# Performance work log

Hardware: AMD Instinct MI355X
Metric: run time of the kernel (lower is better)

## Reference

```python
import jax, jax.numpy as jnp
import numpy as np

CONTEXT = 3  # matches init_kwargs

def _shift_fwd(x, d):
    # out[:, d:, :] = x[:, :-d, :] ; zeros in front
    N = x.shape[1]
    return jnp.pad(x, ((0, 0), (d, 0), (0, 0)))[:, :N, :]

def _shift_bwd(x, d):
    # out[:, :-d, :] = x[:, d:, :] ; zeros at end
    return jnp.pad(x, ((0, 0), (0, d), (0, 0)))[:, d:, :]

def _pairing(x_l, x_r, context):
    if context <= 1:
        return x_l, x_r
    # NB: torch source initializes both lists with x_l (faithful reproduction)
    z_l, z_r = [x_l], [x_l]
    for d in range(1, context // 2 + 1):
        z_l.append(_shift_fwd(x_l, d))   # z_lu
        z_r.append(_shift_bwd(x_r, d))   # z_ru
        z_l.append(_shift_bwd(x_l, d))   # z_ld
        z_r.append(_shift_fwd(x_r, d))   # z_rd
    return jnp.concatenate(z_l, axis=2), jnp.concatenate(z_r, axis=2)

def setup_inputs() -> dict:
    key = jax.random.key(0)
    ks = jax.random.split(key, 8)
    B, N, n_in = 2, 512, 64
    n = n_in * CONTEXT  # 192
    H = 128
    n_out = 8
    s = 0.05
    return {
        "x_l": jax.random.normal(ks[0], (B, N, n_in), jnp.float32),
        "x_r": jax.random.normal(ks[1], (B, N, n_in), jnp.float32),
        "fc_l_W": jax.random.normal(ks[2], (H, n), jnp.float32) * s,
        "fc_l_b": jax.random.normal(ks[3], (H,), jnp.float32) * s,
        "fc_r_W": jax.random.normal(ks[4], (H, n), jnp.float32) * s,
        "fc_r_b": jax.random.normal(ks[5], (H,), jnp.float32) * s,
        "bilinear_W": jax.random.normal(ks[6], (n_out, H, H), jnp.float32) * s,
        "bilinear_b": jax.random.normal(ks[7], (n_out,), jnp.float32) * s,
    }

def reference(x_l, x_r, fc_l_W, fc_l_b, fc_r_W, fc_r_b, bilinear_W, bilinear_b):
    # context-shift pairing: [B,N,n_in] -> [B,N,n_in*context]
    zl, zr = _pairing(x_l, x_r, CONTEXT)
    # per-position MLP with CELU (dropout_rate=0 -> identity)
    hl = jax.nn.celu(jnp.einsum('bnf,hf->bnh', zl, fc_l_W) + fc_l_b)
    hr = jax.nn.celu(jnp.einsum('bnf,hf->bnh', zr, fc_r_W) + fc_r_b)
    # bilinear over the NxN pair grid without materializing [B,N,N,H]:
    # out[b,i,j,o] = hl[b,i] @ W[o] @ hr[b,j] + b[o]
    t = jnp.einsum('bih,ohg->biog', hl, bilinear_W)   # [B,N,n_out,H]
    out = jnp.einsum('biog,bjg->bijo', t, hr) + bilinear_b
    return out  # [B,N,N,n_out]
```

## Files before the change

kernel.cpp:

```cpp
#include <hip/hip_runtime.h>
#include <math.h>

#define BB 2
#define NN 512
#define NIN 64
#define NF 192
#define HH 128
#define NOUT 8

typedef short short8 __attribute__((ext_vector_type(8)));
typedef float f32x4 __attribute__((ext_vector_type(4)));

__device__ __forceinline__ float celu1(float x) {
    return x > 0.0f ? x : expm1f(x);
}

__device__ __forceinline__ ushort f2b(float f) {
    union { float f; uint u; } v; v.f = f;
    uint r = v.u + 0x7fffu + ((v.u >> 16) & 1u);
    return (ushort)(r >> 16);
}
__device__ __forceinline__ uint pack2(float a, float b) {
    return (uint)f2b(a) | ((uint)f2b(b) << 16);
}
__device__ __forceinline__ short8 cvt8(const float* __restrict__ p) {
    float4 a = *(const float4*)p;
    float4 b = *(const float4*)(p + 4);
    union { uint4 u; short8 s; } c;
    c.u.x = pack2(a.x, a.y); c.u.y = pack2(a.z, a.w);
    c.u.z = pack2(b.x, b.y); c.u.w = pack2(b.z, b.w);
    return c.s;
}

__global__ __launch_bounds__(256) void k1_kernel(
    const float* __restrict__ x_l, const float* __restrict__ x_r,
    const float* __restrict__ Wl, const float* __restrict__ bl,
    const float* __restrict__ Wr, const float* __restrict__ br,
    const float* __restrict__ Wb,
    ushort* __restrict__ hl_bf, ushort* __restrict__ hr_bf,
    ushort* __restrict__ Wt)
{
    __shared__ float lds[128 * 65];
    int blk = blockIdx.x;
    int tid = threadIdx.x;

    if (blk < 256) {
        int mb = blk & 63;
        int lr = (blk >> 6) & 1;
        int hh = blk >> 7;
        int m0 = mb * 16;
        int b  = m0 >> 9;
        int i_base = m0 & (NN - 1);

        int wave = tid >> 6;
        int lane = tid & 63;
        int lrow = lane & 15;
        int lgrp = lane >> 4;
        int h0 = hh * 64 + wave * 16;
        int i = i_base + lrow;

        const float* Wm   = lr ? Wr : Wl;
        const float* bias = lr ? br : bl;
        const float* xa   = lr ? x_r : x_l;
        ushort* dst       = lr ? hr_bf : hl_bf;

        short8 bf[6];
        #pragma unroll
        for (int kk = 0; kk < 6; ++kk) {
            int part = kk >> 1;
            int c0 = (kk & 1) * 32 + lgrp * 8;
            int s; const float* src;
            if (part == 0)      { s = 0;            src = x_l; }
            else if (part == 1) { s = lr ? +1 : -1; src = xa; }
            else                { s = lr ? -1 : +1; src = xa; }
            int row = i + s;
            short8 v = (short8)0;
            if ((unsigned)row < (unsigned)NN)
                v = cvt8(&src[(b * NN + row) * NIN + c0]);
            bf[kk] = v;
        }

        f32x4 acc = (f32x4)(0.0f);
        #pragma unroll
        for (int kk = 0; kk < 6; ++kk) {
            short8 afrag = cvt8(&Wm[(h0 + lrow) * NF + kk * 32 + lgrp * 8]);
            acc = __builtin_amdgcn_mfma_f32_16x16x32_bf16(afrag, bf[kk], acc, 0, 0, 0);
        }

        int h_base = h0 + lgrp * 4;
        float4 bv = *(const float4*)&bias[h_base];
        int m = m0 + lrow;
        uint2 v;
        v.x = pack2(celu1(acc[0] + bv.x), celu1(acc[1] + bv.y));
        v.y = pack2(celu1(acc[2] + bv.z), celu1(acc[3] + bv.w));
        *(uint2*)&dst[m * HH + h_base] = v;
    } else {
        int o = blk - 256;
        for (int h0 = 0; h0 < HH; h0 += 64) {
            for (int idx = tid; idx < 64 * 128; idx += 256) {
                int hh = idx >> 7;
                int g  = idx & 127;
                lds[g * 65 + hh] = Wb[(o * HH + h0 + hh) * HH + g];
            }
            __syncthreads();
            for (int idx = tid; idx < 128 * 64; idx += 256) {
                int g  = idx >> 6;
                int hh = idx & 63;
                Wt[(o * HH + g) * HH + h0 + hh] = f2b(lds[g * 65 + hh]);
            }
            __syncthreads();
        }
    }
}

#define TSTR 136

__global__ __launch_bounds__(256) void k2_kernel(
    const ushort* __restrict__ hl_bf, const ushort* __restrict__ hr_bf,
    const ushort* __restrict__ Wt, const float* __restrict__ bias,
    float* __restrict__ out)
{
    __shared__ ushort t_s[128 * TSTR];

    int j0 = blockIdx.x * 128;
    int i0 = blockIdx.y * 16;
    int b  = blockIdx.z;
    int tid  = threadIdx.x;
    int wave = tid >> 6;
    int lane = tid & 63;
    int lrow = lane & 15;
    int lgrp = lane >> 4;

    short8 hfrag[4];
    #pragma unroll
    for (int kk = 0; kk < 4; ++kk)
        hfrag[kk] = *(const short8*)&hl_bf[(b * NN + i0 + lrow) * HH + kk * 32 + lgrp * 8];

    #pragma unroll
    for (int o = 0; o < NOUT; ++o) {
        #pragma unroll
        for (int gt = 0; gt < 2; ++gt) {
            int g_base = wave * 32 + gt * 16;
            f32x4 acc = (f32x4)(0.0f);
            #pragma unroll
            for (int kk = 0; kk < 4; ++kk) {
                short8 afrag = *(const short8*)&Wt[(o * HH + g_base + lrow) * HH + kk * 32 + lgrp * 8];
                acc = __builtin_amdgcn_mfma_f32_16x16x32_bf16(afrag, hfrag[kk], acc, 0, 0, 0);
            }
            int m  = lrow * 8 + o;
            int gg = g_base + lgrp * 4;
            uint2 v;
            v.x = pack2(acc[0], acc[1]);
            v.y = pack2(acc[2], acc[3]);
            *(uint2*)&t_s[m * TSTR + gg] = v;
        }
    }
    __syncthreads();

    int jw = j0 + wave * 32;

    f32x4 acc2[8][2];
    #pragma unroll
    for (int ms = 0; ms < 8; ++ms)
        #pragma unroll
        for (int jt = 0; jt < 2; ++jt) acc2[ms][jt] = (f32x4)(0.0f);

    const ushort* hb = hr_bf + (size_t)b * NN * HH;

    #pragma unroll
    for (int kk = 0; kk < 4; ++kk) {
        int koff = kk * 32 + lgrp * 8;
        short8 bfr[2];
        #pragma unroll
        for (int jt = 0; jt < 2; ++jt)
            bfr[jt] = *(const short8*)&hb[(jw + jt * 16 + lrow) * HH + koff];
        #pragma unroll
        for (int ms = 0; ms < 8; ++ms) {
            short8 afr = *(const short8*)&t_s[(ms * 16 + lrow) * TSTR + koff];
            #pragma unroll
            for (int jt = 0; jt < 2; ++jt)
                acc2[ms][jt] = __builtin_amdgcn_mfma_f32_16x16x32_bf16(afr, bfr[jt], acc2[ms][jt], 0, 0, 0);
        }
    }

    float4 b0 = *(const float4*)&bias[0];
    float4 b1 = *(const float4*)&bias[4];

    #pragma unroll
    for (int ms = 0; ms < 8; ++ms) {
        int m_base = ms * 16 + lgrp * 4;
        int i  = i0 + (m_base >> 3);
        int o0 = m_base & 7;
        float4 bv = o0 ? b1 : b0;
        #pragma unroll
        for (int jt = 0; jt < 2; ++jt) {
            int j = jw + jt * 16 + lrow;
            float4 v;
            v.x = acc2[ms][jt][0] + bv.x;
            v.y = acc2[ms][jt][1] + bv.y;
            v.z = acc2[ms][jt][2] + bv.z;
            v.w = acc2[ms][jt][3] + bv.w;
            float* dst = out + ((size_t)((b * NN + i) * NN + j)) * NOUT + o0;
            *(float4*)dst = v;
        }
    }
}

extern "C" void kernel_launch(void* const* d_in, const int* in_sizes, int n_in,
                              void* d_out, int out_size, void* d_ws, size_t ws_size,
                              hipStream_t stream) {
    const float* x_l  = (const float*)d_in[0];
    const float* x_r  = (const float*)d_in[1];
    const float* Wl   = (const float*)d_in[2];
    const float* bl   = (const float*)d_in[3];
    const float* Wr   = (const float*)d_in[4];
    const float* br   = (const float*)d_in[5];
    const float* Wb   = (const float*)d_in[6];
    const float* bb   = (const float*)d_in[7];
    float* out = (float*)d_out;

    ushort* hl_bf = (ushort*)d_ws;
    ushort* hr_bf = hl_bf + BB * NN * HH;
    ushort* Wt    = hr_bf + BB * NN * HH;

    k1_kernel<<<264, 256, 0, stream>>>(x_l, x_r, Wl, bl, Wr, br, Wb,
                                       hl_bf, hr_bf, Wt);
    k2_kernel<<<dim3(NN / 128, NN / 16, BB), 256, 0, stream>>>(
        hl_bf, hr_bf, Wt, bb, out);
}
```

Measured before the change: 26.72 us.

## Use 1024-thread blocks in k2 with one 16x16 output tile per wave

```diff
diff --git a/kernel.cpp b/kernel.cpp
--- a/kernel.cpp
+++ b/kernel.cpp
@@ -115,7 +115,7 @@
 
 #define TSTR 136
 
-__global__ __launch_bounds__(256) void k2_kernel(
+__global__ __launch_bounds__(1024) void k2_kernel(
     const ushort* __restrict__ hl_bf, const ushort* __restrict__ hr_bf,
     const ushort* __restrict__ Wt, const float* __restrict__ bias,
     float* __restrict__ out)
@@ -131,77 +131,63 @@
     int lrow = lane & 15;
     int lgrp = lane >> 4;
 
+    int jt = wave & 7;
+    int jw = j0 + jt * 16;
+    const ushort* hb = hr_bf + (size_t)b * NN * HH;
+    short8 bfr[4];
+    #pragma unroll
+    for (int kk = 0; kk < 4; ++kk)
+        bfr[kk] = *(const short8*)&hb[(jw + lrow) * HH + kk * 32 + lgrp * 8];
+
     short8 hfrag[4];
     #pragma unroll
     for (int kk = 0; kk < 4; ++kk)
         hfrag[kk] = *(const short8*)&hl_bf[(b * NN + i0 + lrow) * HH + kk * 32 + lgrp * 8];
 
-    #pragma unroll
-    for (int o = 0; o < NOUT; ++o) {
-        #pragma unroll
-        for (int gt = 0; gt < 2; ++gt) {
-            int g_base = wave * 32 + gt * 16;
-            f32x4 acc = (f32x4)(0.0f);
-            #pragma unroll
-            for (int kk = 0; kk < 4; ++kk) {
-                short8 afrag = *(const short8*)&Wt[(o * HH + g_base + lrow) * HH + kk * 32 + lgrp * 8];
-                acc = __builtin_amdgcn_mfma_f32_16x16x32_bf16(afrag, hfrag[kk], acc, 0, 0, 0);
-            }
-            int m  = lrow * 8 + o;
-            int gg = g_base + lgrp * 4;
-            uint2 v;
-            v.x = pack2(acc[0], acc[1]);
-            v.y = pack2(acc[2], acc[3]);
-            *(uint2*)&t_s[m * TSTR + gg] = v;
-        }
+    int o_p1 = wave >> 1;
+    int gh   = wave & 1;
+    #pragma unroll
+    for (int gt = 0; gt < 4; ++gt) {
+        int g_base = gh * 64 + gt * 16;
+        f32x4 acc = (f32x4)(0.0f);
+        #pragma unroll
+        for (int kk = 0; kk < 4; ++kk) {
+            short8 afrag = *(const short8*)&Wt[(o_p1 * HH + g_base + lrow) * HH + kk * 32 + lgrp * 8];
+            acc = __builtin_amdgcn_mfma_f32_16x16x32_bf16(afrag, hfrag[kk], acc, 0, 0, 0);
+        }
+        int row = o_p1 * 16 + lrow;
+        int gg = g_base + lgrp * 4;
+        uint2 v;
+        v.x = pack2(acc[0], acc[1]);
+        v.y = pack2(acc[2], acc[3]);
+        *(uint2*)&t_s[row * TSTR + gg] = v;
     }
     __syncthreads();
 
-    int jw = j0 + wave * 32;
-
-    f32x4 acc2[8][2];
-    #pragma unroll
-    for (int ms = 0; ms < 8; ++ms)
-        #pragma unroll
-        for (int jt = 0; jt < 2; ++jt) acc2[ms][jt] = (f32x4)(0.0f);
-
-    const ushort* hb = hr_bf + (size_t)b * NN * HH;
+    int og = (wave >> 3) * 4;
+    f32x4 acc2[4];
+    #pragma unroll
+    for (int s = 0; s < 4; ++s) acc2[s] = (f32x4)(0.0f);
 
     #pragma unroll
     for (int kk = 0; kk < 4; ++kk) {
         int koff = kk * 32 + lgrp * 8;
-        short8 bfr[2];
-        #pragma unroll
-        for (int jt = 0; jt < 2; ++jt)
-            bfr[jt] = *(const short8*)&hb[(jw + jt * 16 + lrow) * HH + koff];
-        #pragma unroll
-        for (int ms = 0; ms < 8; ++ms) {
-            short8 afr = *(const short8*)&t_s[(ms * 16 + lrow) * TSTR + koff];
-            #pragma unroll
-            for (int jt = 0; jt < 2; ++jt)
-                acc2[ms][jt] = __builtin_amdgcn_mfma_f32_16x16x32_bf16(afr, bfr[jt], acc2[ms][jt], 0, 0, 0);
-        }
-    }
-
-    float4 b0 = *(const float4*)&bias[0];
-    float4 b1 = *(const float4*)&bias[4];
-
-    #pragma unroll
-    for (int ms = 0; ms < 8; ++ms) {
-        int m_base = ms * 16 + lgrp * 4;
-        int i  = i0 + (m_base >> 3);
-        int o0 = m_base & 7;
-        float4 bv = o0 ? b1 : b0;
-        #pragma unroll
-        for (int jt = 0; jt < 2; ++jt) {
-            int j = jw + jt * 16 + lrow;
-            float4 v;
-            v.x = acc2[ms][jt][0] + bv.x;
-            v.y = acc2[ms][jt][1] + bv.y;
-            v.z = acc2[ms][jt][2] + bv.z;
-            v.w = acc2[ms][jt][3] + bv.w;
-            float* dst = out + ((size_t)((b * NN + i) * NN + j)) * NOUT + o0;
-            *(float4*)dst = v;
+        #pragma unroll
+        for (int s = 0; s < 4; ++s) {
+            short8 afr = *(const short8*)&t_s[((og + s) * 16 + lrow) * TSTR + koff];
+            acc2[s] = __builtin_amdgcn_mfma_f32_16x16x32_bf16(afr, bfr[kk], acc2[s], 0, 0, 0);
+        }
+    }
+
+    int j = jw + lrow;
+    #pragma unroll
+    for (int s = 0; s < 4; ++s) {
+        int o = og + s;
+        float bv = bias[o];
+        #pragma unroll
+        for (int r = 0; r < 4; ++r) {
+            int i = i0 + lgrp * 4 + r;
+            out[((size_t)((b * NN + i) * NN + j)) * NOUT + o] = acc2[s][r] + bv;
         }
     }
 }
@@ -225,6 +211,6 @@
 
     k1_kernel<<<264, 256, 0, stream>>>(x_l, x_r, Wl, bl, Wr, br, Wb,
                                        hl_bf, hr_bf, Wt);
-    k2_kernel<<<dim3(NN / 128, NN / 16, BB), 256, 0, stream>>>(
+    k2_kernel<<<dim3(NN / 128, NN / 16, BB), 1024, 0, stream>>>(
         hl_bf, hr_bf, Wt, bb, out);
 }
```

New measurement: 33.24 us. 24.4% more time.

## Split bilinear stage into separate t-projection and output GEMM kernels

Applied to the files above, without the earlier changes.

```diff
diff --git a/kernel.cpp b/kernel.cpp
--- a/kernel.cpp
+++ b/kernel.cpp
@@ -113,93 +113,108 @@
     }
 }
 
-#define TSTR 136
-
-__global__ __launch_bounds__(256) void k2_kernel(
-    const ushort* __restrict__ hl_bf, const ushort* __restrict__ hr_bf,
-    const ushort* __restrict__ Wt, const float* __restrict__ bias,
-    float* __restrict__ out)
+__global__ __launch_bounds__(256) void t_kernel(
+    const ushort* __restrict__ hl_bf, const ushort* __restrict__ Wt,
+    ushort* __restrict__ t_bf)
 {
-    __shared__ ushort t_s[128 * TSTR];
-
-    int j0 = blockIdx.x * 128;
-    int i0 = blockIdx.y * 16;
-    int b  = blockIdx.z;
+    int o  = blockIdx.y;
+    int m0 = blockIdx.x * 64;
     int tid  = threadIdx.x;
     int wave = tid >> 6;
     int lane = tid & 63;
     int lrow = lane & 15;
     int lgrp = lane >> 4;
 
-    short8 hfrag[4];
-    #pragma unroll
-    for (int kk = 0; kk < 4; ++kk)
-        hfrag[kk] = *(const short8*)&hl_bf[(b * NN + i0 + lrow) * HH + kk * 32 + lgrp * 8];
-
-    #pragma unroll
-    for (int o = 0; o < NOUT; ++o) {
-        #pragma unroll
-        for (int gt = 0; gt < 2; ++gt) {
-            int g_base = wave * 32 + gt * 16;
-            f32x4 acc = (f32x4)(0.0f);
-            #pragma unroll
-            for (int kk = 0; kk < 4; ++kk) {
-                short8 afrag = *(const short8*)&Wt[(o * HH + g_base + lrow) * HH + kk * 32 + lgrp * 8];
-                acc = __builtin_amdgcn_mfma_f32_16x16x32_bf16(afrag, hfrag[kk], acc, 0, 0, 0);
-            }
-            int m  = lrow * 8 + o;
-            int gg = g_base + lgrp * 4;
-            uint2 v;
-            v.x = pack2(acc[0], acc[1]);
-            v.y = pack2(acc[2], acc[3]);
-            *(uint2*)&t_s[m * TSTR + gg] = v;
-        }
-    }
-    __syncthreads();
-
-    int jw = j0 + wave * 32;
-
-    f32x4 acc2[8][2];
-    #pragma unroll
-    for (int ms = 0; ms < 8; ++ms)
-        #pragma unroll
-        for (int jt = 0; jt < 2; ++jt) acc2[ms][jt] = (f32x4)(0.0f);
-
-    const ushort* hb = hr_bf + (size_t)b * NN * HH;
+    int m_wave = m0 + wave * 16;
+
+    f32x4 acc[8];
+    #pragma unroll
+    for (int gt = 0; gt < 8; ++gt) acc[gt] = (f32x4)(0.0f);
+
+    const ushort* Wo = Wt + o * HH * HH;
 
     #pragma unroll
     for (int kk = 0; kk < 4; ++kk) {
         int koff = kk * 32 + lgrp * 8;
-        short8 bfr[2];
+        short8 a[8];
+        #pragma unroll
+        for (int gt = 0; gt < 8; ++gt)
+            a[gt] = *(const short8*)&Wo[(gt * 16 + lrow) * HH + koff];
+        short8 bfrag = *(const short8*)&hl_bf[(m_wave + lrow) * HH + koff];
+        #pragma unroll
+        for (int gt = 0; gt < 8; ++gt)
+            acc[gt] = __builtin_amdgcn_mfma_f32_16x16x32_bf16(a[gt], bfrag, acc[gt], 0, 0, 0);
+    }
+
+    int m = m_wave + lrow;
+    #pragma unroll
+    for (int gt = 0; gt < 8; ++gt) {
+        int g0 = gt * 16 + lgrp * 4;
+        uint lo = (uint)f2b(acc[gt][0]) | ((uint)f2b(acc[gt][1]) << 16);
+        uint hi = (uint)f2b(acc[gt][2]) | ((uint)f2b(acc[gt][3]) << 16);
+        uint2 v; v.x = lo; v.y = hi;
+        *(uint2*)&t_bf[(m * NOUT + o) * HH + g0] = v;
+    }
+}
+
+__global__ __launch_bounds__(256) void out_kernel(
+    const ushort* __restrict__ t_bf, const ushort* __restrict__ hr_bf,
+    const float* __restrict__ bias, float* __restrict__ out)
+{
+    int b  = blockIdx.z;
+    int m0 = blockIdx.y * 64;
+    int j0 = blockIdx.x * 128;
+    int tid  = threadIdx.x;
+    int wave = tid >> 6;
+    int lane = tid & 63;
+    int lrow = lane & 15;
+    int lgrp = lane >> 4;
+
+    int jw = j0 + wave * 32;
+
+    f32x4 acc[4][2];
+    #pragma unroll
+    for (int mt = 0; mt < 4; ++mt)
+        #pragma unroll
+        for (int jt = 0; jt < 2; ++jt) acc[mt][jt] = (f32x4)(0.0f);
+
+    const ushort* tb = t_bf + (size_t)b * (NN * NOUT) * HH;
+    const ushort* hb = hr_bf + (size_t)b * NN * HH;
+
+    #pragma unroll
+    for (int kk = 0; kk < 4; ++kk) {
+        int koff = kk * 32 + lgrp * 8;
+        short8 a[4], bf[2];
+        #pragma unroll
+        for (int mt = 0; mt < 4; ++mt)
+            a[mt] = *(const short8*)&tb[(m0 + mt * 16 + lrow) * HH + koff];
         #pragma unroll
         for (int jt = 0; jt < 2; ++jt)
-            bfr[jt] = *(const short8*)&hb[(jw + jt * 16 + lrow) * HH + koff];
-        #pragma unroll
-        for (int ms = 0; ms < 8; ++ms) {
-            short8 afr = *(const short8*)&t_s[(ms * 16 + lrow) * TSTR + koff];
+            bf[jt] = *(const short8*)&hb[(jw + jt * 16 + lrow) * HH + koff];
+        #pragma unroll
+        for (int mt = 0; mt < 4; ++mt)
             #pragma unroll
             for (int jt = 0; jt < 2; ++jt)
-                acc2[ms][jt] = __builtin_amdgcn_mfma_f32_16x16x32_bf16(afr, bfr[jt], acc2[ms][jt], 0, 0, 0);
-        }
+                acc[mt][jt] = __builtin_amdgcn_mfma_f32_16x16x32_bf16(a[mt], bf[jt], acc[mt][jt], 0, 0, 0);
     }
 
     float4 b0 = *(const float4*)&bias[0];
     float4 b1 = *(const float4*)&bias[4];
 
     #pragma unroll
-    for (int ms = 0; ms < 8; ++ms) {
-        int m_base = ms * 16 + lgrp * 4;
-        int i  = i0 + (m_base >> 3);
+    for (int mt = 0; mt < 4; ++mt) {
+        int m_base = m0 + mt * 16 + lgrp * 4;
+        int i  = m_base >> 3;
         int o0 = m_base & 7;
         float4 bv = o0 ? b1 : b0;
         #pragma unroll
         for (int jt = 0; jt < 2; ++jt) {
             int j = jw + jt * 16 + lrow;
             float4 v;
-            v.x = acc2[ms][jt][0] + bv.x;
-            v.y = acc2[ms][jt][1] + bv.y;
-            v.z = acc2[ms][jt][2] + bv.z;
-            v.w = acc2[ms][jt][3] + bv.w;
+            v.x = acc[mt][jt][0] + bv.x;
+            v.y = acc[mt][jt][1] + bv.y;
+            v.z = acc[mt][jt][2] + bv.z;
+            v.w = acc[mt][jt][3] + bv.w;
             float* dst = out + ((size_t)((b * NN + i) * NN + j)) * NOUT + o0;
             *(float4*)dst = v;
         }
@@ -222,9 +237,11 @@
     ushort* hl_bf = (ushort*)d_ws;
     ushort* hr_bf = hl_bf + BB * NN * HH;
     ushort* Wt    = hr_bf + BB * NN * HH;
+    ushort* t_bf  = Wt + NOUT * HH * HH;
 
     k1_kernel<<<264, 256, 0, stream>>>(x_l, x_r, Wl, bl, Wr, br, Wb,
                                        hl_bf, hr_bf, Wt);
-    k2_kernel<<<dim3(NN / 128, NN / 16, BB), 256, 0, stream>>>(
-        hl_bf, hr_bf, Wt, bb, out);
-}
+    t_kernel<<<dim3(16, NOUT), 256, 0, stream>>>(hl_bf, Wt, t_bf);
+    out_kernel<<<dim3(NN / 128, 4096 / 64, BB), 256, 0, stream>>>(
+        t_bf, hr_bf, bb, out);
+}
```

New measurement: 29.60 us. 1.11x slower.
